# Kernel optimization log

Measured on AMD Instinct MI355X. Metric: run time of the kernel, lower is better.

Reference implementation:

```python
import jax, jax.numpy as jnp
import numpy as np

B, T, IN_DIM, OUT_DIM = 1024, 64, 8, 2
H, K, HIDDEN = 3, 5, 256
LOG_STD_MIN, LOG_STD_MAX = -20.0, 2.0


def setup_inputs() -> dict:
    key = jax.random.key(0)
    ks = jax.random.split(key, 12)
    def lin(k, fan_in, fan_out):
        b = 1.0 / np.sqrt(fan_in)
        return jax.random.uniform(k, (fan_in, fan_out), jnp.float32, -b, b)
    inp = {
        'state': jax.random.normal(ks[0], (B, T, IN_DIM), jnp.float32),
        'noise': jax.random.normal(ks[1], (B, T, OUT_DIM), jnp.float32),
        'Wq': lin(ks[2], IN_DIM, K * H),
        'Wk': lin(ks[3], K, K * H),
        'Wv': lin(ks[4], K, K * H),
        'W1': lin(ks[5], K * H + IN_DIM, HIDDEN),
        'b1': jnp.zeros((HIDDEN,), jnp.float32),
        'W2': lin(ks[6], HIDDEN, HIDDEN),
        'b2': jnp.zeros((HIDDEN,), jnp.float32),
        'Wmu': jax.random.uniform(ks[7], (HIDDEN, OUT_DIM), jnp.float32, -0.003, 0.003),
        'bmu': jax.random.uniform(ks[8], (OUT_DIM,), jnp.float32, -0.003, 0.003),
        'Wls': jax.random.uniform(ks[9], (HIDDEN, OUT_DIM), jnp.float32, -0.003, 0.003),
        'bls': jax.random.uniform(ks[10], (OUT_DIM,), jnp.float32, -0.003, 0.003),
    }
    return inp


# static off-diagonal neighbor indices: row i -> all j != i
_OFFDIAG = np.array([[j for j in range(T) if j != i] for i in range(T)], dtype=np.int32)


def _forward(state, noise, Wq, Wk, Wv, W1, b1, W2, b2, Wmu, bmu, Wls, bls):
    b, t, _ = state.shape
    # rel[b,i,j] = state[b,j,:4] - state[b,i,:4]
    rel4 = state[:, None, :, 0:4] - state[:, :, None, 0:4]          # [b,t,t,4] (x,y,vx,vy)
    x_comp = rel4[..., 0::2]                                         # [x, vx]
    y_comp = rel4[..., 1::2]                                         # [y, vy]
    ang = (-state[:, :, 7] + 0.5 * jnp.pi)[:, None, :, None]         # varies with j (own-ref of key agent)
    c, s = jnp.cos(ang), jnp.sin(ang)
    xn = x_comp * c - y_comp * s                                     # [x', vx']
    yn = x_comp * s + y_comp * c                                     # [y', vy']
    rel = jnp.stack([xn[..., 0], yn[..., 0], xn[..., 1], yn[..., 1]], axis=-1)  # [b,t,t,4]
    # drop self-pairs (diagonal) -> [b,t,t-1,4]
    idx = jnp.asarray(_OFFDIAG)
    rel_od = rel[:, jnp.arange(t)[:, None], idx]
    r = jnp.sqrt(rel_od[..., 0] ** 2 + rel_od[..., 1] ** 2)[..., None]   # [b,t,t-1,1]
    r_trans = jax.nn.sigmoid(1.0 - 5.0 * (r - 0.2))                       # 1/(1+exp(-1+5(r-0.2)))
    rel_n = jnp.concatenate([rel_od[..., 0:2] / r, rel_od[..., 2:4], r_trans], axis=-1)  # [b,t,t-1,5]
    h, k = H, K
    q = (state @ Wq).reshape(b, t, h, k)                              # [b,t,h,k]
    keys = (rel_n @ Wk).reshape(b, t, t - 1, h, k)                    # [b,t,n,h,k]
    vals = (rel_n @ Wv).reshape(b, t, t - 1, h, k)
    scores = jnp.einsum('btnhk,bthk->bthn', keys, q) / jnp.sqrt(jnp.float32(k))
    w = jax.nn.softmax(scores, axis=-1)                               # over t-1 neighbors
    att = jnp.einsum('bthn,btnhk->bthk', w, vals).reshape(b, t, h * k)
    x = jnp.concatenate([att, state], axis=-1)
    x = jax.nn.relu(x @ W1 + b1)
    x = jax.nn.relu(x @ W2 + b2)
    mu = jnp.tanh(x @ Wmu + bmu)
    log_std = jnp.tanh(x @ Wls + bls)
    log_std = LOG_STD_MIN + 0.5 * (LOG_STD_MAX - LOG_STD_MIN) * (log_std + 1.0)
    std = jnp.exp(log_std)
    z = mu + std * noise                                              # rsample with explicit noise
    action = jnp.tanh(z)
    # Normal(mu,std).log_prob(z) with (z-mu)/std == noise
    log_prob = -0.5 * noise ** 2 - log_std - 0.5 * jnp.log(2.0 * jnp.pi)
    log_prob = log_prob - jnp.log(1.0 - action ** 2 + 1e-7)
    log_prob = jnp.sum(log_prob, axis=-1, keepdims=True)
    return action, log_prob


def reference(state, noise, Wq, Wk, Wv, W1, b1, W2, b2, Wmu, bmu, Wls, bls):
    return _forward(state, noise, Wq, Wk, Wv, W1, b1, W2, b2, Wmu, bmu, Wls, bls)
```

## Files before the change

kernel.cpp:

```cpp
#include <hip/hip_runtime.h>
#include <math.h>

#define NROWS 65536

typedef short bf16x8 __attribute__((ext_vector_type(8)));
typedef float f32x4  __attribute__((ext_vector_type(4)));
typedef float f32x2  __attribute__((ext_vector_type(2)));

__device__ __forceinline__ unsigned short f2bf(float x){
    unsigned int u = __float_as_uint(x);
    u += 0x7FFFu + ((u >> 16) & 1u);
    return (unsigned short)(u >> 16);
}
__device__ __forceinline__ f32x2 sp2(float x){ return (f32x2){x, x}; }

template<int CTRL, int RM>
__device__ __forceinline__ float dpp_add(float v){
    int m = __builtin_amdgcn_update_dpp(0, __float_as_int(v), CTRL, RM, 0xF, 1);
    return v + __int_as_float(m);
}
__device__ __forceinline__ float rowsum16(float v){
    v = dpp_add<0x111, 0xF>(v);
    v = dpp_add<0x112, 0xF>(v);
    v = dpp_add<0x114, 0xF>(v);
    v = dpp_add<0x118, 0xF>(v);
    return v;
}
__device__ __forceinline__ float bfly8_add(float v){
    v = dpp_add<0xB1, 0xF>(v);
    v = dpp_add<0x4E, 0xF>(v);
    v = dpp_add<0x141, 0xF>(v);
    return v;
}

__global__ __launch_bounds__(256) void prep_kernel(
    const float* __restrict__ W2, const float* __restrict__ W1,
    unsigned short* __restrict__ w2frag, unsigned short* __restrict__ w1frag)
{
    const int bx = blockIdx.x, t = threadIdx.x;
    if (bx < 128){
        const int ct = bx >> 3, kk = bx & 7;
        #pragma unroll
        for (int s = 0; s < 2; ++s){
            int f = t * 2 + s;
            int lane = f >> 3, e = f & 7;
            int k = kk * 32 + (lane >> 4) * 8 + e;
            int c = ct * 16 + (lane & 15);
            w2frag[(size_t)(ct * 8 + kk) * 512 + f] = f2bf(W2[k * 256 + c]);
        }
    } else {
        #pragma unroll
        for (int s = 0; s < 32; ++s){
            int flat = t * 32 + s;
            int ct = flat >> 9, r = flat & 511;
            int lane = r >> 3, e = r & 7;
            int k = (lane >> 4) * 8 + e;
            int c = ct * 16 + (lane & 15);
            w1frag[flat] = (k < 23) ? f2bf(W1[k * 256 + c]) : (unsigned short)0;
        }
    }
}

__global__ __launch_bounds__(512, 4) void actor_kernel(
    const float* __restrict__ state, const float* __restrict__ noise,
    const float* __restrict__ Wq, const float* __restrict__ Wk,
    const float* __restrict__ Wv,
    const unsigned short* __restrict__ w1frag, const float* __restrict__ b1,
    const unsigned short* __restrict__ w2frag, const float* __restrict__ b2,
    const float* __restrict__ Wmu, const float* __restrict__ bmu,
    const float* __restrict__ Wls, const float* __restrict__ bls,
    float* __restrict__ action_out, float* __restrict__ logprob_out)
{
    __shared__ __align__(16) unsigned char uniA[64 * 264 * 2];
    float* sLDS  = (float*)uniA;
    float* pjLDS = sLDS + 576;
    float* qkLDS = pjLDS + 384;
    unsigned short* h1LDS = (unsigned short*)uniA;
    __shared__ __align__(16) unsigned short x0LDS[64 * 40];
    __shared__ float headLDS[8 * 64 * 5];

    const int t    = threadIdx.x;
    const int lane = t & 63;
    const int w    = t >> 6;
    const int lm   = lane & 15;
    const int lq   = lane >> 4;
    const int b    = blockIdx.x;

    {
        float v = state[(size_t)b * 512 + t];
        int r = t >> 3, c = t & 7;
        sLDS[r * 9 + c] = v;
        if (c < 4) pjLDS[(r & 31) * 12 + c * 2 + (r >> 5)] = v;
    }
    __syncthreads();

    if (t < 192){
        const int row = t & 63, h = t >> 6;
        float s[8];
        #pragma unroll
        for (int d = 0; d < 8; ++d) s[d] = sLDS[row * 9 + d];
        float q[5];
        #pragma unroll
        for (int e = 0; e < 5; ++e){
            int m = h * 5 + e;
            float acc = 0.f;
            #pragma unroll
            for (int d = 0; d < 8; ++d) acc += s[d] * Wq[d * 15 + m];
            q[e] = acc;
        }
        #pragma unroll
        for (int f = 0; f < 5; ++f){
            float acc = 0.f;
            #pragma unroll
            for (int kk = 0; kk < 5; ++kk) acc += Wk[f * 15 + h * 5 + kk] * q[kk];
            qkLDS[row * 17 + h * 5 + f] = acc * 0.64519834f;
        }
    } else if (w == 7){
        const int row = lane;
        float ang = 1.5707963267948966f - sLDS[row * 9 + 7];
        float sn, cs;
        __sincosf(ang, &sn, &cs);
        int base = (row & 31) * 12 + (row >> 5);
        pjLDS[base + 8]  = sn;
        pjLDS[base + 10] = cs;
    }
    __syncthreads();

    {
        const int il = lane >> 3;
        const int js = lane & 7;
        const int i  = w * 8 + il;
        const float si0 = sLDS[i * 9 + 0], si1 = sLDS[i * 9 + 1];
        const float si2 = sLDS[i * 9 + 2], si3 = sLDS[i * 9 + 3];
        float qkv[15];
        #pragma unroll
        for (int m = 0; m < 15; ++m) qkv[m] = qkLDS[i * 17 + m];

        f32x2 s0 = {0.f,0.f}, s1 = {0.f,0.f}, s2 = {0.f,0.f};
        f32x2 g0[5], g1[5], g2[5];
        #pragma unroll
        for (int f = 0; f < 5; ++f){ g0[f] = sp2(0.f); g1[f] = sp2(0.f); g2[f] = sp2(0.f); }

        #pragma unroll
        for (int jj = 0; jj < 4; ++jj){
            const int jb = jj * 8 + js;
            const f32x2* pp = (const f32x2*)&pjLDS[jb * 12];
            f32x2 p0 = pp[0], p1 = pp[1], p2 = pp[2], p3 = pp[3];
            f32x2 sn = pp[4], cs = pp[5];
            f32x2 d0 = p0 - sp2(si0), d1 = p1 - sp2(si1);
            f32x2 d2 = p2 - sp2(si2), d3 = p3 - sp2(si3);
            f32x2 xn0 = d0 * cs - d1 * sn, yn0 = d0 * sn + d1 * cs;
            f32x2 xn1 = d2 * cs - d3 * sn, yn1 = d2 * sn + d3 * cs;
            f32x2 r2v = xn0 * xn0 + yn0 * yn0;
            const bool self0 = (jb == i), self1 = (jb + 32 == i);
            f32x2 inv_r;
            inv_r.x = self0 ? 0.f : rsqrtf(r2v.x);
            inv_r.y = self1 ? 0.f : rsqrtf(r2v.y);
            f32x2 rv  = r2v * inv_r;
            f32x2 arg = rv * sp2(7.2134752f) - sp2(2.8853901f);
            f32x2 ex; ex.x = exp2f(arg.x); ex.y = exp2f(arg.y);
            f32x2 f4; f4.x = 1.f / (1.f + ex.x); f4.y = 1.f / (1.f + ex.y);
            f32x2 f0 = xn0 * inv_r, f1 = yn0 * inv_r;
            f32x2 sc0 = f0*sp2(qkv[0])  + f1*sp2(qkv[1])  + xn1*sp2(qkv[2])  + yn1*sp2(qkv[3])  + f4*sp2(qkv[4]);
            f32x2 sc1 = f0*sp2(qkv[5])  + f1*sp2(qkv[6])  + xn1*sp2(qkv[7])  + yn1*sp2(qkv[8])  + f4*sp2(qkv[9]);
            f32x2 sc2 = f0*sp2(qkv[10]) + f1*sp2(qkv[11]) + xn1*sp2(qkv[12]) + yn1*sp2(qkv[13]) + f4*sp2(qkv[14]);
            f32x2 e0, e1, e2;
            e0.x = self0 ? 0.f : exp2f(sc0.x);  e0.y = self1 ? 0.f : exp2f(sc0.y);
            e1.x = self0 ? 0.f : exp2f(sc1.x);  e1.y = self1 ? 0.f : exp2f(sc1.y);
            e2.x = self0 ? 0.f : exp2f(sc2.x);  e2.y = self1 ? 0.f : exp2f(sc2.y);
            s0 += e0; s1 += e1; s2 += e2;
            g0[0] += e0*f0; g0[1] += e0*f1; g0[2] += e0*xn1; g0[3] += e0*yn1; g0[4] += e0*f4;
            g1[0] += e1*f0; g1[1] += e1*f1; g1[2] += e1*xn1; g1[3] += e1*yn1; g1[4] += e1*f4;
            g2[0] += e2*f0; g2[1] += e2*f1; g2[2] += e2*xn1; g2[3] += e2*yn1; g2[4] += e2*f4;
        }
        float S0 = s0.x + s0.y, S1 = s1.x + s1.y, S2 = s2.x + s2.y;
        float G0[5], G1[5], G2[5];
        #pragma unroll
        for (int f = 0; f < 5; ++f){
            G0[f] = bfly8_add(g0[f].x + g0[f].y);
            G1[f] = bfly8_add(g1[f].x + g1[f].y);
            G2[f] = bfly8_add(g2[f].x + g2[f].y);
        }
        S0 = bfly8_add(S0); S1 = bfly8_add(S1); S2 = bfly8_add(S2);
        float i0 = 1.f / S0, i1 = 1.f / S1, i2 = 1.f / S2;

        #pragma unroll
        for (int mm = 0; mm < 2; ++mm){
            int m = js * 2 + mm;
            if (m < 15){
                float A0 = (m < 5) ? G0[0] : (m < 10) ? G1[0] : G2[0];
                float A1 = (m < 5) ? G0[1] : (m < 10) ? G1[1] : G2[1];
                float A2 = (m < 5) ? G0[2] : (m < 10) ? G1[2] : G2[2];
                float A3 = (m < 5) ? G0[3] : (m < 10) ? G1[3] : G2[3];
                float A4 = (m < 5) ? G0[4] : (m < 10) ? G1[4] : G2[4];
                float I  = (m < 5) ? i0    : (m < 10) ? i1    : i2;
                float av = (A0 * Wv[m] + A1 * Wv[15 + m] + A2 * Wv[30 + m]
                          + A3 * Wv[45 + m] + A4 * Wv[60 + m]) * I;
                x0LDS[i * 40 + m] = f2bf(av);
            }
        }
        x0LDS[i * 40 + 15 + js] = f2bf(sLDS[i * 9 + js]);
        x0LDS[i * 40 + 23 + js] = 0;
        if (js == 0) x0LDS[i * 40 + 31] = 0;
    }
    __syncthreads();

    {
        bf16x8 afr[4];
        #pragma unroll
        for (int rt = 0; rt < 4; ++rt)
            afr[rt] = *(const bf16x8*)&x0LDS[(rt * 16 + lm) * 40 + lq * 8];
        #pragma unroll
        for (int ci = 0; ci < 2; ++ci){
            const int ct = w * 2 + ci;
            bf16x8 bfr = *(const bf16x8*)&w1frag[(size_t)ct * 512 + lane * 8];
            float bb = b1[ct * 16 + lm];
            #pragma unroll
            for (int rt = 0; rt < 4; ++rt){
                f32x4 c0 = {0.f, 0.f, 0.f, 0.f};
                c0 = __builtin_amdgcn_mfma_f32_16x16x32_bf16(afr[rt], bfr, c0, 0, 0, 0);
                #pragma unroll
                for (int p = 0; p < 4; ++p)
                    h1LDS[(rt * 16 + lq * 4 + p) * 264 + ct * 16 + lm] = f2bf(fmaxf(c0[p] + bb, 0.f));
            }
        }
    }
    __syncthreads();

    {
        f32x4 acc[4][2];
        #pragma unroll
        for (int rt = 0; rt < 4; ++rt)
            #pragma unroll
            for (int ci = 0; ci < 2; ++ci) acc[rt][ci] = (f32x4){0.f, 0.f, 0.f, 0.f};

        #pragma unroll
        for (int kk = 0; kk < 8; ++kk){
            bf16x8 arf[4], brf[2];
            #pragma unroll
            for (int rt = 0; rt < 4; ++rt)
                arf[rt] = *(const bf16x8*)&h1LDS[(rt * 16 + lm) * 264 + kk * 32 + lq * 8];
            #pragma unroll
            for (int ci = 0; ci < 2; ++ci)
                brf[ci] = *(const bf16x8*)&w2frag[(size_t)((w * 2 + ci) * 8 + kk) * 512 + lane * 8];
            #pragma unroll
            for (int rt = 0; rt < 4; ++rt)
                #pragma unroll
                for (int ci = 0; ci < 2; ++ci)
                    acc[rt][ci] = __builtin_amdgcn_mfma_f32_16x16x32_bf16(arf[rt], brf[ci], acc[rt][ci], 0, 0, 0);
        }

        float bb[2];
        float2 wm[2], wl[2];
        #pragma unroll
        for (int ci = 0; ci < 2; ++ci){
            int c = (w * 2 + ci) * 16 + lm;
            bb[ci] = b2[c];
            wm[ci] = *(const float2*)&Wmu[c * 2];
            wl[ci] = *(const float2*)&Wls[c * 2];
        }
        #pragma unroll
        for (int rt = 0; rt < 4; ++rt){
            #pragma unroll
            for (int p = 0; p < 4; ++p){
                float m0 = 0.f, m1 = 0.f, l0 = 0.f, l1 = 0.f;
                #pragma unroll
                for (int ci = 0; ci < 2; ++ci){
                    float hv = fmaxf(acc[rt][ci][p] + bb[ci], 0.f);
                    m0 += hv * wm[ci].x;
                    m1 += hv * wm[ci].y;
                    l0 += hv * wl[ci].x;
                    l1 += hv * wl[ci].y;
                }
                m0 = rowsum16(m0); m1 = rowsum16(m1);
                l0 = rowsum16(l0); l1 = rowsum16(l1);
                if (lm == 15){
                    int row = rt * 16 + lq * 4 + p;
                    float* hp = &headLDS[(w * 64 + row) * 5];
                    hp[0] = m0; hp[1] = m1; hp[2] = l0; hp[3] = l1;
                }
            }
        }
    }
    __syncthreads();

    if (t < 64){
        const int row = t;
        float m0 = 0.f, m1 = 0.f, l0 = 0.f, l1 = 0.f;
        #pragma unroll
        for (int ww = 0; ww < 8; ++ww){
            const float* hp = &headLDS[(ww * 64 + row) * 5];
            m0 += hp[0]; m1 += hp[1]; l0 += hp[2]; l1 += hp[3];
        }
        const size_t grow = (size_t)b * 64 + row;
        float n0 = noise[grow * 2 + 0];
        float n1 = noise[grow * 2 + 1];
        float lp = 0.f;
        {
            float mu = tanhf(m0 + bmu[0]);
            float ls = tanhf(l0 + bls[0]);
            ls = -20.f + 11.f * (ls + 1.f);
            float sd = expf(ls);
            float a = tanhf(mu + sd * n0);
            action_out[grow * 2 + 0] = a;
            lp += -0.5f * n0 * n0 - ls - 0.9189385332046727f - logf(1.f - a * a + 1e-7f);
        }
        {
            float mu = tanhf(m1 + bmu[1]);
            float ls = tanhf(l1 + bls[1]);
            ls = -20.f + 11.f * (ls + 1.f);
            float sd = expf(ls);
            float a = tanhf(mu + sd * n1);
            action_out[grow * 2 + 1] = a;
            lp += -0.5f * n1 * n1 - ls - 0.9189385332046727f - logf(1.f - a * a + 1e-7f);
        }
        logprob_out[grow] = lp;
    }
}

extern "C" void kernel_launch(void* const* d_in, const int* in_sizes, int n_in,
                              void* d_out, int out_size, void* d_ws, size_t ws_size,
                              hipStream_t stream)
{
    (void)in_sizes; (void)n_in; (void)out_size; (void)ws_size;
    const float* state = (const float*)d_in[0];
    const float* noise = (const float*)d_in[1];
    const float* Wq  = (const float*)d_in[2];
    const float* Wk  = (const float*)d_in[3];
    const float* Wv  = (const float*)d_in[4];
    const float* W1  = (const float*)d_in[5];
    const float* b1  = (const float*)d_in[6];
    const float* W2  = (const float*)d_in[7];
    const float* b2  = (const float*)d_in[8];
    const float* Wmu = (const float*)d_in[9];
    const float* bmu = (const float*)d_in[10];
    const float* Wls = (const float*)d_in[11];
    const float* bls = (const float*)d_in[12];

    unsigned short* w2frag = (unsigned short*)d_ws;
    unsigned short* w1frag = w2frag + 65536;

    float* action_out  = (float*)d_out;
    float* logprob_out = (float*)d_out + (size_t)NROWS * 2;

    prep_kernel<<<129, 256, 0, stream>>>(W2, W1, w2frag, w1frag);
    actor_kernel<<<1024, 512, 0, stream>>>(state, noise, Wq, Wk, Wv,
        w1frag, b1, w2frag, b2, Wmu, bmu, Wls, bls, action_out, logprob_out);
}
```

Baseline: 119.9 us.

## Split each batch element across two blocks of 32 query rows

```diff
diff --git a/kernel.cpp b/kernel.cpp
--- a/kernel.cpp
+++ b/kernel.cpp
@@ -26,10 +26,11 @@
     v = dpp_add<0x118, 0xF>(v);
     return v;
 }
-__device__ __forceinline__ float bfly8_add(float v){
+__device__ __forceinline__ float bfly16_add(float v){
     v = dpp_add<0xB1, 0xF>(v);
     v = dpp_add<0x4E, 0xF>(v);
     v = dpp_add<0x141, 0xF>(v);
+    v = dpp_add<0x140, 0xF>(v);
     return v;
 }
 
@@ -71,20 +72,21 @@
     const float* __restrict__ Wls, const float* __restrict__ bls,
     float* __restrict__ action_out, float* __restrict__ logprob_out)
 {
-    __shared__ __align__(16) unsigned char uniA[64 * 264 * 2];
+    __shared__ __align__(16) unsigned char uniA[32 * 264 * 2];
     float* sLDS  = (float*)uniA;
     float* pjLDS = sLDS + 576;
     float* qkLDS = pjLDS + 384;
     unsigned short* h1LDS = (unsigned short*)uniA;
-    __shared__ __align__(16) unsigned short x0LDS[64 * 40];
-    __shared__ float headLDS[8 * 64 * 5];
-
-    const int t    = threadIdx.x;
-    const int lane = t & 63;
-    const int w    = t >> 6;
-    const int lm   = lane & 15;
-    const int lq   = lane >> 4;
-    const int b    = blockIdx.x;
+    __shared__ __align__(16) unsigned short x0LDS[32 * 40];
+    __shared__ float headLDS[8 * 32 * 5];
+
+    const int t     = threadIdx.x;
+    const int lane  = t & 63;
+    const int w     = t >> 6;
+    const int lm    = lane & 15;
+    const int lq    = lane >> 4;
+    const int b     = blockIdx.x >> 1;
+    const int ibase = (blockIdx.x & 1) * 32;
 
     {
         float v = state[(size_t)b * 512 + t];
@@ -94,8 +96,9 @@
     }
     __syncthreads();
 
-    if (t < 192){
-        const int row = t & 63, h = t >> 6;
+    if (t < 96){
+        const int rloc = t & 31, h = t >> 5;
+        const int row = ibase + rloc;
         float s[8];
         #pragma unroll
         for (int d = 0; d < 8; ++d) s[d] = sLDS[row * 9 + d];
@@ -113,10 +116,10 @@
             float acc = 0.f;
             #pragma unroll
             for (int kk = 0; kk < 5; ++kk) acc += Wk[f * 15 + h * 5 + kk] * q[kk];
-            qkLDS[row * 17 + h * 5 + f] = acc * 0.64519834f;
-        }
-    } else if (w == 7){
-        const int row = lane;
+            qkLDS[rloc * 17 + h * 5 + f] = acc * 0.64519834f;
+        }
+    } else if (t < 160){
+        const int row = t - 96;
         float ang = 1.5707963267948966f - sLDS[row * 9 + 7];
         float sn, cs;
         __sincosf(ang, &sn, &cs);
@@ -127,14 +130,13 @@
     __syncthreads();
 
     {
-        const int il = lane >> 3;
-        const int js = lane & 7;
-        const int i  = w * 8 + il;
+        const int iloc = w * 4 + lq;
+        const int i    = ibase + iloc;
         const float si0 = sLDS[i * 9 + 0], si1 = sLDS[i * 9 + 1];
         const float si2 = sLDS[i * 9 + 2], si3 = sLDS[i * 9 + 3];
         float qkv[15];
         #pragma unroll
-        for (int m = 0; m < 15; ++m) qkv[m] = qkLDS[i * 17 + m];
+        for (int m = 0; m < 15; ++m) qkv[m] = qkLDS[iloc * 17 + m];
 
         f32x2 s0 = {0.f,0.f}, s1 = {0.f,0.f}, s2 = {0.f,0.f};
         f32x2 g0[5], g1[5], g2[5];
@@ -142,8 +144,8 @@
         for (int f = 0; f < 5; ++f){ g0[f] = sp2(0.f); g1[f] = sp2(0.f); g2[f] = sp2(0.f); }
 
         #pragma unroll
-        for (int jj = 0; jj < 4; ++jj){
-            const int jb = jj * 8 + js;
+        for (int jj = 0; jj < 2; ++jj){
+            const int jb = jj * 16 + lm;
             const f32x2* pp = (const f32x2*)&pjLDS[jb * 12];
             f32x2 p0 = pp[0], p1 = pp[1], p2 = pp[2], p3 = pp[3];
             f32x2 sn = pp[4], cs = pp[5];
@@ -173,42 +175,38 @@
             g1[0] += e1*f0; g1[1] += e1*f1; g1[2] += e1*xn1; g1[3] += e1*yn1; g1[4] += e1*f4;
             g2[0] += e2*f0; g2[1] += e2*f1; g2[2] += e2*xn1; g2[3] += e2*yn1; g2[4] += e2*f4;
         }
-        float S0 = s0.x + s0.y, S1 = s1.x + s1.y, S2 = s2.x + s2.y;
+        float S0 = bfly16_add(s0.x + s0.y);
+        float S1 = bfly16_add(s1.x + s1.y);
+        float S2 = bfly16_add(s2.x + s2.y);
         float G0[5], G1[5], G2[5];
         #pragma unroll
         for (int f = 0; f < 5; ++f){
-            G0[f] = bfly8_add(g0[f].x + g0[f].y);
-            G1[f] = bfly8_add(g1[f].x + g1[f].y);
-            G2[f] = bfly8_add(g2[f].x + g2[f].y);
-        }
-        S0 = bfly8_add(S0); S1 = bfly8_add(S1); S2 = bfly8_add(S2);
+            G0[f] = bfly16_add(g0[f].x + g0[f].y);
+            G1[f] = bfly16_add(g1[f].x + g1[f].y);
+            G2[f] = bfly16_add(g2[f].x + g2[f].y);
+        }
         float i0 = 1.f / S0, i1 = 1.f / S1, i2 = 1.f / S2;
 
-        #pragma unroll
-        for (int mm = 0; mm < 2; ++mm){
-            int m = js * 2 + mm;
-            if (m < 15){
-                float A0 = (m < 5) ? G0[0] : (m < 10) ? G1[0] : G2[0];
-                float A1 = (m < 5) ? G0[1] : (m < 10) ? G1[1] : G2[1];
-                float A2 = (m < 5) ? G0[2] : (m < 10) ? G1[2] : G2[2];
-                float A3 = (m < 5) ? G0[3] : (m < 10) ? G1[3] : G2[3];
-                float A4 = (m < 5) ? G0[4] : (m < 10) ? G1[4] : G2[4];
-                float I  = (m < 5) ? i0    : (m < 10) ? i1    : i2;
-                float av = (A0 * Wv[m] + A1 * Wv[15 + m] + A2 * Wv[30 + m]
-                          + A3 * Wv[45 + m] + A4 * Wv[60 + m]) * I;
-                x0LDS[i * 40 + m] = f2bf(av);
-            }
-        }
-        x0LDS[i * 40 + 15 + js] = f2bf(sLDS[i * 9 + js]);
-        x0LDS[i * 40 + 23 + js] = 0;
-        if (js == 0) x0LDS[i * 40 + 31] = 0;
+        if (lm < 15){
+            float A0 = (lm < 5) ? G0[0] : (lm < 10) ? G1[0] : G2[0];
+            float A1 = (lm < 5) ? G0[1] : (lm < 10) ? G1[1] : G2[1];
+            float A2 = (lm < 5) ? G0[2] : (lm < 10) ? G1[2] : G2[2];
+            float A3 = (lm < 5) ? G0[3] : (lm < 10) ? G1[3] : G2[3];
+            float A4 = (lm < 5) ? G0[4] : (lm < 10) ? G1[4] : G2[4];
+            float I  = (lm < 5) ? i0    : (lm < 10) ? i1    : i2;
+            float av = (A0 * Wv[lm] + A1 * Wv[15 + lm] + A2 * Wv[30 + lm]
+                      + A3 * Wv[45 + lm] + A4 * Wv[60 + lm]) * I;
+            x0LDS[iloc * 40 + lm] = f2bf(av);
+        }
+        if (lm < 8) x0LDS[iloc * 40 + 15 + lm] = f2bf(sLDS[i * 9 + lm]);
+        if (lm < 9) x0LDS[iloc * 40 + 23 + lm] = 0;
     }
     __syncthreads();
 
     {
-        bf16x8 afr[4];
-        #pragma unroll
-        for (int rt = 0; rt < 4; ++rt)
+        bf16x8 afr[2];
+        #pragma unroll
+        for (int rt = 0; rt < 2; ++rt)
             afr[rt] = *(const bf16x8*)&x0LDS[(rt * 16 + lm) * 40 + lq * 8];
         #pragma unroll
         for (int ci = 0; ci < 2; ++ci){
@@ -216,7 +214,7 @@
             bf16x8 bfr = *(const bf16x8*)&w1frag[(size_t)ct * 512 + lane * 8];
             float bb = b1[ct * 16 + lm];
             #pragma unroll
-            for (int rt = 0; rt < 4; ++rt){
+            for (int rt = 0; rt < 2; ++rt){
                 f32x4 c0 = {0.f, 0.f, 0.f, 0.f};
                 c0 = __builtin_amdgcn_mfma_f32_16x16x32_bf16(afr[rt], bfr, c0, 0, 0, 0);
                 #pragma unroll
@@ -228,23 +226,23 @@
     __syncthreads();
 
     {
-        f32x4 acc[4][2];
-        #pragma unroll
-        for (int rt = 0; rt < 4; ++rt)
+        f32x4 acc[2][2];
+        #pragma unroll
+        for (int rt = 0; rt < 2; ++rt)
             #pragma unroll
             for (int ci = 0; ci < 2; ++ci) acc[rt][ci] = (f32x4){0.f, 0.f, 0.f, 0.f};
 
         #pragma unroll
         for (int kk = 0; kk < 8; ++kk){
-            bf16x8 arf[4], brf[2];
-            #pragma unroll
-            for (int rt = 0; rt < 4; ++rt)
+            bf16x8 arf[2], brf[2];
+            #pragma unroll
+            for (int rt = 0; rt < 2; ++rt)
                 arf[rt] = *(const bf16x8*)&h1LDS[(rt * 16 + lm) * 264 + kk * 32 + lq * 8];
             #pragma unroll
             for (int ci = 0; ci < 2; ++ci)
                 brf[ci] = *(const bf16x8*)&w2frag[(size_t)((w * 2 + ci) * 8 + kk) * 512 + lane * 8];
             #pragma unroll
-            for (int rt = 0; rt < 4; ++rt)
+            for (int rt = 0; rt < 2; ++rt)
                 #pragma unroll
                 for (int ci = 0; ci < 2; ++ci)
                     acc[rt][ci] = __builtin_amdgcn_mfma_f32_16x16x32_bf16(arf[rt], brf[ci], acc[rt][ci], 0, 0, 0);
@@ -260,7 +258,7 @@
             wl[ci] = *(const float2*)&Wls[c * 2];
         }
         #pragma unroll
-        for (int rt = 0; rt < 4; ++rt){
+        for (int rt = 0; rt < 2; ++rt){
             #pragma unroll
             for (int p = 0; p < 4; ++p){
                 float m0 = 0.f, m1 = 0.f, l0 = 0.f, l1 = 0.f;
@@ -276,7 +274,7 @@
                 l0 = rowsum16(l0); l1 = rowsum16(l1);
                 if (lm == 15){
                     int row = rt * 16 + lq * 4 + p;
-                    float* hp = &headLDS[(w * 64 + row) * 5];
+                    float* hp = &headLDS[(w * 32 + row) * 5];
                     hp[0] = m0; hp[1] = m1; hp[2] = l0; hp[3] = l1;
                 }
             }
@@ -284,15 +282,15 @@
     }
     __syncthreads();
 
-    if (t < 64){
+    if (t < 32){
         const int row = t;
         float m0 = 0.f, m1 = 0.f, l0 = 0.f, l1 = 0.f;
         #pragma unroll
         for (int ww = 0; ww < 8; ++ww){
-            const float* hp = &headLDS[(ww * 64 + row) * 5];
+            const float* hp = &headLDS[(ww * 32 + row) * 5];
             m0 += hp[0]; m1 += hp[1]; l0 += hp[2]; l1 += hp[3];
         }
-        const size_t grow = (size_t)b * 64 + row;
+        const size_t grow = (size_t)b * 64 + ibase + row;
         float n0 = noise[grow * 2 + 0];
         float n1 = noise[grow * 2 + 1];
         float lp = 0.f;
@@ -344,6 +342,6 @@
     float* logprob_out = (float*)d_out + (size_t)NROWS * 2;
 
     prep_kernel<<<129, 256, 0, stream>>>(W2, W1, w2frag, w1frag);
-    actor_kernel<<<1024, 512, 0, stream>>>(state, noise, Wq, Wk, Wv,
+    actor_kernel<<<2048, 512, 0, stream>>>(state, noise, Wq, Wk, Wv,
         w1frag, b1, w2frag, b2, Wmu, bmu, Wls, bls, action_out, logprob_out);
 }
```

After: 122.4 us. 2.1% more time.
